# Kernel optimization log

Hardware: AMD Instinct MI355X
Metric: run time of the kernel (lower is better)

The kernel has to match this reference:

```python
import jax, jax.numpy as jnp
import numpy as np
import math

# Model dims (match init_kwargs)
H = 4096      # hidden_size
NH = 32       # num attention heads
NKV = 8       # num kv heads
D = 128       # head_dim
S = 2048      # num tokens
WINDOW = 1024 # sliding window (layer_idx=0 -> active)
SCALE = D ** -0.5
# YaRN rope params from GptOssConfig.rope_parameters
BASE = 500000.0
FACTOR = 4.0
ORIG_MAX = 32768
BETA_FAST = 32
BETA_SLOW = 1


def _yarn_cos_sin(positions):
    """YaRN-scaled rotary cos/sin, NEOX style. Returns ([S, D/2], [S, D/2])."""
    d2 = D // 2
    pos_freqs = BASE ** (np.arange(d2, dtype=np.float64) * 2.0 / D)
    inv_extra = 1.0 / pos_freqs
    inv_inter = 1.0 / (FACTOR * pos_freqs)

    def corr_dim(n):
        return (D * math.log(ORIG_MAX / (n * 2 * math.pi))) / (2 * math.log(BASE))

    low = max(math.floor(corr_dim(BETA_FAST)), 0)
    high = min(math.ceil(corr_dim(BETA_SLOW)), d2 - 1)
    ramp = np.clip((np.arange(d2, dtype=np.float64) - low) / max(high - low, 0.001), 0.0, 1.0)
    mask = 1.0 - ramp  # 1 -> extrapolation (high freq), 0 -> interpolation (low freq)
    inv_freq = inv_inter * (1.0 - mask) + inv_extra * mask
    mscale = 0.1 * math.log(FACTOR) + 1.0
    freqs = positions.astype(jnp.float32)[:, None] * jnp.asarray(inv_freq, dtype=jnp.float32)[None, :]
    return jnp.cos(freqs) * mscale, jnp.sin(freqs) * mscale


def _rope(x, cos, sin):
    # x: [S, h, D]; rotate-halves (NEOX)
    x1, x2 = jnp.split(x, 2, axis=-1)
    c, s = cos[:, None, :], sin[:, None, :]
    return jnp.concatenate([x1 * c - x2 * s, x2 * c + x1 * s], axis=-1)


def reference(hidden_states, positions, qkv_w, qkv_b, o_w, o_b, sinks):
    qs, kvs = NH * D, NKV * D
    qkv = hidden_states @ qkv_w.T + qkv_b                  # [S, qs + 2*kvs]
    q = qkv[:, :qs].reshape(S, NH, D)
    k = qkv[:, qs:qs + kvs].reshape(S, NKV, D)
    v = qkv[:, qs + kvs:].reshape(S, NKV, D)

    cos, sin = _yarn_cos_sin(positions)
    q = _rope(q, cos, sin)
    k = _rope(k, cos, sin)

    # GQA: expand kv heads to match q heads
    g = NH // NKV
    k = jnp.repeat(k, g, axis=1)                            # [S, NH, D]
    v = jnp.repeat(v, g, axis=1)

    scores = jnp.einsum('qhd,khd->hqk', q, k) * SCALE       # [NH, S, S]
    i = jnp.arange(S)[:, None]
    j = jnp.arange(S)[None, :]
    allowed = (j <= i) & ((i - j) < WINDOW)                 # causal + sliding window
    scores = jnp.where(allowed[None, :, :], scores, -jnp.inf)

    # sink-aware softmax: learned per-head sink logit joins the normalization
    m = jnp.maximum(jnp.max(scores, axis=-1), sinks[:, None])   # [NH, S]
    e = jnp.exp(scores - m[..., None])                          # masked -> exp(-inf)=0
    denom = e.sum(-1) + jnp.exp(sinks[:, None] - m)             # [NH, S]
    probs = e / denom[..., None]

    attn = jnp.einsum('hqk,khd->qhd', probs, v).reshape(S, NH * D)
    return attn @ o_w.T + o_b


def setup_inputs() -> dict:
    key = jax.random.key(0)
    k1, k2, k3, k4, k5 = jax.random.split(key, 5)
    w_scale = 0.02
    return {
        'hidden_states': jax.random.normal(k1, (S, H), dtype=jnp.float32),
        'positions': jnp.arange(S, dtype=jnp.int64) if jax.config.jax_enable_x64 else jnp.arange(S, dtype=jnp.int32),
        'qkv_w': jax.random.normal(k2, (NH * D + 2 * NKV * D, H), dtype=jnp.float32) * w_scale,
        'qkv_b': jax.random.normal(k3, (NH * D + 2 * NKV * D,), dtype=jnp.float32) * w_scale,
        'o_w': jax.random.normal(k4, (H, H), dtype=jnp.float32) * w_scale,
        'o_b': jax.random.normal(k5, (H,), dtype=jnp.float32) * w_scale,
        'sinks': jnp.zeros((NH,), dtype=jnp.float32),
    }
```

## Files before the change

kernel.cpp:

```cpp
#include <hip/hip_runtime.h>

#define S_LEN   2048
#define HID     4096
#define NH      32
#define NKV     8
#define HD      128
#define QKV_N   (NH*HD + 2*NKV*HD)
#define WINDOW  1024

typedef unsigned short u16;
typedef short s8v  __attribute__((ext_vector_type(8)));
typedef short s4v  __attribute__((ext_vector_type(4)));
typedef float f4v  __attribute__((ext_vector_type(4)));

#define MFMA16x32(a, b, c) __builtin_amdgcn_mfma_f32_16x16x32_bf16(a, b, c, 0, 0, 0)

typedef __attribute__((address_space(1))) const unsigned int g_u32;
typedef __attribute__((address_space(3))) unsigned int l_u32;

__device__ __forceinline__ float bf2f(u16 h) {
  union { unsigned int u; float f; } x;
  x.u = ((unsigned int)h) << 16;
  return x.f;
}
__device__ __forceinline__ u16 f2bf(float f) {
  union { float f; unsigned int u; } x;
  x.f = f;
  unsigned int u = x.u;
  return (u16)((u + 0x7FFFu + ((u >> 16) & 1u)) >> 16);
}

__global__ __launch_bounds__(256) void cvt_bf16(const float* __restrict__ in,
                                               u16* __restrict__ out) {
  int i = (blockIdx.x * 256 + threadIdx.x) * 4;
  float4 v = *(const float4*)&in[i];
  u16 h[4] = { f2bf(v.x), f2bf(v.y), f2bf(v.z), f2bf(v.w) };
  *(s4v*)&out[i] = *(const s4v*)h;
}

template<int OUT_BF16>
__global__ __launch_bounds__(512, 2) void gemm_bt(
    const u16* __restrict__ A, const u16* __restrict__ B,
    const float* __restrict__ bias, void* __restrict__ Cp,
    int M, int N, int K)
{
  __shared__ __align__(16) char lds[3 * 49152];
  const int tid  = threadIdx.x;
  const int lane = tid & 63;
  const int w    = tid >> 6;
  const int wm   = w >> 2, wn = w & 3;
  const int ln   = lane & 15, quad = lane >> 4;
  const long mBase = (long)blockIdx.y * 128;
  const long nBase = (long)blockIdx.x * 256;
  const u16* Ab = A + mBase * (long)K;
  const u16* Bb = B + nBase * (long)K;
  const long rs = (long)K * 2;

  f4v acc[4][4];
#pragma unroll
  for (int i = 0; i < 4; ++i)
#pragma unroll
    for (int j = 0; j < 4; ++j)
#pragma unroll
      for (int r = 0; r < 4; ++r) acc[i][j][r] = 0.0f;

  const int nt = K >> 6;

  auto stage = [&](int tile) {
    char* base = lds + (tile % 3) * 49152;
    const int ktb = tile * 128;
#pragma unroll
    for (int k = 0; k < 6; ++k) {
      const u16* gsrc = (k < 2) ? Ab : Bb;
      char* ldst      = (k < 2) ? base : (base + 16384);
      const int kk    = (k < 2) ? k : (k - 2);
      int o  = kk * 8192 + w * 1024 + lane * 16;
      int o2 = o ^ ((o >> 3) & 0x70);
      const char* gp = (const char*)gsrc + (long)(o2 >> 7) * rs + ktb + (o2 & 127);
      __builtin_amdgcn_global_load_lds((g_u32*)(const void*)gp,
                                       (l_u32*)(void*)(ldst + kk * 8192 + w * 1024),
                                       16, 0, 0);
    }
  };

  stage(0);
  stage(1);
  asm volatile("s_waitcnt vmcnt(6)" ::: "memory");
  __builtin_amdgcn_s_barrier();
  __builtin_amdgcn_sched_barrier(0);

  int bsel = 0;
  for (int t = 0; t < nt; ++t) {
    char* base = lds + bsel * 49152;
    if (t + 2 < nt) stage(t + 2);

    __builtin_amdgcn_s_setprio(1);
#pragma unroll
    for (int ks = 0; ks < 2; ++ks) {
      s8v af[4], bf[4];
#pragma unroll
      for (int f = 0; f < 4; ++f) {
        int r = wm * 64 + f * 16 + ln;
        int o = r * 128 + ks * 64 + quad * 16;
        o ^= (r & 7) << 4;
        af[f] = *(const s8v*)(base + o);
      }
#pragma unroll
      for (int j = 0; j < 4; ++j) {
        int r = wn * 64 + j * 16 + ln;
        int o = r * 128 + ks * 64 + quad * 16;
        o ^= (r & 7) << 4;
        bf[j] = *(const s8v*)(base + 16384 + o);
      }
#pragma unroll
      for (int i = 0; i < 4; ++i)
#pragma unroll
        for (int j = 0; j < 4; ++j)
          acc[i][j] = MFMA16x32(af[i], bf[j], acc[i][j]);
    }
    __builtin_amdgcn_s_setprio(0);

    if (t < nt - 2) {
      asm volatile("s_waitcnt vmcnt(6)" ::: "memory");
      __builtin_amdgcn_s_barrier();
      __builtin_amdgcn_sched_barrier(0);
    } else if (t == nt - 2) {
      asm volatile("s_waitcnt vmcnt(0)" ::: "memory");
      __builtin_amdgcn_s_barrier();
      __builtin_amdgcn_sched_barrier(0);
    }
    bsel = (bsel == 2) ? 0 : bsel + 1;
  }

#pragma unroll
  for (int i = 0; i < 4; ++i) {
    long rowb = mBase + wm * 64 + i * 16 + quad * 4;
#pragma unroll
    for (int j = 0; j < 4; ++j) {
      long col = nBase + wn * 64 + j * 16 + ln;
      float bv = bias[col];
#pragma unroll
      for (int r = 0; r < 4; ++r) {
        float v = acc[i][j][r] + bv;
        if (OUT_BF16) ((u16*)Cp)[(rowb + r) * (long)N + col] = f2bf(v);
        else          ((float*)Cp)[(rowb + r) * (long)N + col] = v;
      }
    }
  }
}

__global__ __launch_bounds__(256) void rope_split(
    const u16* __restrict__ qkv, const int* __restrict__ positions,
    u16* __restrict__ qo, u16* __restrict__ ko, u16* __restrict__ vo)
{
  const int s = blockIdx.x;
  const int t = threadIdx.x;
  __shared__ float csh[64], snh[64];

  if (t < 64) {
    const double LN_BASE = log(500000.0);
    const double TWO_PI  = 6.283185307179586476925287;
    double cf  = 128.0 * log(32768.0 / (32.0 * TWO_PI)) / (2.0 * LN_BASE);
    double cs_ = 128.0 * log(32768.0 / TWO_PI) / (2.0 * LN_BASE);
    double lowd  = floor(cf);  if (lowd < 0.0)  lowd = 0.0;
    double highd = ceil(cs_);  if (highd > 63.0) highd = 63.0;
    double denom = highd - lowd; if (denom < 0.001) denom = 0.001;
    double d = (double)t;
    double inv_extra = exp(-LN_BASE * d / 64.0);
    double inv_inter = inv_extra * 0.25;
    double ramp = (d - lowd) / denom;
    ramp = ramp < 0.0 ? 0.0 : (ramp > 1.0 ? 1.0 : ramp);
    double maskv = 1.0 - ramp;
    double invf = inv_inter * (1.0 - maskv) + inv_extra * maskv;
    float freq = (float)positions[s] * (float)invf;
    const float msc = 1.1386294361119891f;
    csh[t] = cosf(freq) * msc;
    snh[t] = sinf(freq) * msc;
  }
  __syncthreads();

  const u16* row = qkv + (size_t)s * QKV_N;
  const float SC = 0.08838834764831845f;

#pragma unroll
  for (int i = 0; i < 8; ++i) {
    int p = i * 256 + t;
    int hh = p >> 6, d = p & 63;
    float x1 = bf2f(row[hh * 128 + d]), x2 = bf2f(row[hh * 128 + d + 64]);
    float c = csh[d], sn = snh[d];
    qo[(size_t)s * 4096 + hh * 128 + d]      = f2bf((x1 * c - x2 * sn) * SC);
    qo[(size_t)s * 4096 + hh * 128 + d + 64] = f2bf((x2 * c + x1 * sn) * SC);
  }
#pragma unroll
  for (int i = 0; i < 2; ++i) {
    int p = i * 256 + t;
    int hh = p >> 6, d = p & 63;
    float x1 = bf2f(row[4096 + hh * 128 + d]), x2 = bf2f(row[4096 + hh * 128 + d + 64]);
    float c = csh[d], sn = snh[d];
    ko[(size_t)s * 1024 + hh * 128 + d]      = f2bf(x1 * c - x2 * sn);
    ko[(size_t)s * 1024 + hh * 128 + d + 64] = f2bf(x2 * c + x1 * sn);
  }
#pragma unroll
  for (int i = 0; i < 4; ++i) {
    int e = i * 256 + t;
    vo[(size_t)s * 1024 + e] = row[5120 + e];
  }
}

__global__ __launch_bounds__(256) void transpose_v(const u16* __restrict__ vb,
                                                   u16* __restrict__ vt) {
  __shared__ u16 tile[64][72];
  const int s0 = blockIdx.x * 64, c0 = blockIdx.y * 64;
  const int tid = threadIdx.x;
#pragma unroll
  for (int t = 0; t < 2; ++t) {
    int row = t * 32 + (tid >> 3), col = (tid & 7) * 8;
    *(s8v*)&tile[row][col] = *(const s8v*)&vb[(size_t)(s0 + row) * 1024 + c0 + col];
  }
  __syncthreads();
#pragma unroll
  for (int t = 0; t < 2; ++t) {
    int orow = t * 32 + (tid >> 3), ocol = (tid & 7) * 8;
    u16 v[8];
#pragma unroll
    for (int e = 0; e < 8; ++e) v[e] = tile[ocol + e][orow];
    *(s8v*)&vt[(size_t)(c0 + orow) * 2048 + s0 + ocol] = *(const s8v*)v;
  }
}

__global__ __launch_bounds__(256) void attn_fwd(
    const u16* __restrict__ Q, const u16* __restrict__ Kb,
    const u16* __restrict__ Vt, const float* __restrict__ sinks,
    u16* __restrict__ O)
{
  const int h = blockIdx.y, kvh = h >> 2;
  const int q0 = blockIdx.x * 64;
  const int tid = threadIdx.x, w = tid >> 6, lane = tid & 63;
  const int ln = lane & 15, quad = lane >> 4;
  const int qw = q0 + w * 16;
  const int qi = qw + ln;

  __shared__ __align__(16) u16 sK[64 * 136];
  __shared__ __align__(16) u16 sVt[128 * 72];
  __shared__ __align__(16) u16 sP[4][16 * 72];

  s8v qf[4];
  {
    const u16* qrow = Q + (size_t)qi * 4096 + h * 128;
#pragma unroll
    for (int kb = 0; kb < 4; ++kb)
      qf[kb] = *(const s8v*)&qrow[kb * 32 + quad * 8];
  }

  float m_v = sinks[h], l_v = 1.0f;
  f4v accO[8];
#pragma unroll
  for (int j = 0; j < 8; ++j)
#pragma unroll
    for (int r = 0; r < 4; ++r) accO[j][r] = 0.0f;

  int lo = q0 - (WINDOW - 1); if (lo < 0) lo = 0; lo &= ~63;

  for (int kt = lo; kt <= q0; kt += 64) {
    __syncthreads();
#pragma unroll
    for (int t = 0; t < 4; ++t) {
      int c = t * 256 + tid;
      int row = c >> 4, col = (c & 15) * 8;
      *(s8v*)&sK[row * 136 + col] =
          *(const s8v*)&Kb[(size_t)(kt + row) * 1024 + kvh * 128 + col];
    }
#pragma unroll
    for (int t = 0; t < 4; ++t) {
      int c = t * 256 + tid;
      int row = c >> 3, col = (c & 7) * 8;
      *(s8v*)&sVt[row * 72 + col] =
          *(const s8v*)&Vt[(size_t)(kvh * 128 + row) * 2048 + kt + col];
    }
    __syncthreads();

    f4v sc[4];
    bool dead[4];
#pragma unroll
    for (int h4 = 0; h4 < 4; ++h4) {
      const int kb16 = kt + h4 * 16;
      dead[h4] = (kb16 > qw + 15) || (kb16 + 15 < qw - (WINDOW - 1));
      if (dead[h4]) {
#pragma unroll
        for (int r = 0; r < 4; ++r) sc[h4][r] = -1e30f;
        continue;
      }
      f4v s;
#pragma unroll
      for (int r = 0; r < 4; ++r) s[r] = 0.0f;
#pragma unroll
      for (int kb = 0; kb < 4; ++kb) {
        s8v kf = *(const s8v*)&sK[(h4 * 16 + ln) * 136 + kb * 32 + quad * 8];
        s = MFMA16x32(kf, qf[kb], s);
      }
      const bool full = (kb16 + 15 <= qw) && (qw + 15 - kb16 <= WINDOW - 1);
      if (!full) {
        int base = qi - kb16 - quad * 4;
#pragma unroll
        for (int r = 0; r < 4; ++r)
          s[r] = ((unsigned)(base - r) <= (WINDOW - 1)) ? s[r] : -1e30f;
      }
      sc[h4] = s;
    }

    float mn = m_v;
#pragma unroll
    for (int h4 = 0; h4 < 4; ++h4)
#pragma unroll
      for (int r = 0; r < 4; ++r) mn = fmaxf(mn, sc[h4][r]);
    mn = fmaxf(mn, __shfl_xor(mn, 16));
    mn = fmaxf(mn, __shfl_xor(mn, 32));

    float alpha = __expf(m_v - mn);
    m_v = mn;
    l_v *= alpha;
#pragma unroll
    for (int j = 0; j < 8; ++j)
#pragma unroll
      for (int r = 0; r < 4; ++r) accO[j][r] *= alpha;

    float lsum = 0.0f;
#pragma unroll
    for (int h4 = 0; h4 < 4; ++h4) {
      float p[4];
#pragma unroll
      for (int r = 0; r < 4; ++r) p[r] = __expf(sc[h4][r] - mn);
      lsum += (p[0] + p[1]) + (p[2] + p[3]);
      u16 pb[4] = { f2bf(p[0]), f2bf(p[1]), f2bf(p[2]), f2bf(p[3]) };
      *(s4v*)&sP[w][ln * 72 + h4 * 16 + quad * 4] = *(const s4v*)pb;
    }
    lsum += __shfl_xor(lsum, 16);
    lsum += __shfl_xor(lsum, 32);
    l_v += lsum;

    __syncthreads();

#pragma unroll
    for (int c2 = 0; c2 < 2; ++c2) {
      if (dead[2 * c2] && dead[2 * c2 + 1]) continue;
      s8v pf = *(const s8v*)&sP[w][ln * 72 + c2 * 32 + quad * 8];
#pragma unroll
      for (int j = 0; j < 8; ++j) {
        s8v vf = *(const s8v*)&sVt[(j * 16 + ln) * 72 + c2 * 32 + quad * 8];
        accO[j] = MFMA16x32(vf, pf, accO[j]);
      }
    }
  }

  __syncthreads();
  u16* sO = sK;
  const float rl = 1.0f / l_v;
#pragma unroll
  for (int j = 0; j < 8; ++j) {
    u16 ob[4] = { f2bf(accO[j][0] * rl), f2bf(accO[j][1] * rl),
                  f2bf(accO[j][2] * rl), f2bf(accO[j][3] * rl) };
    *(s4v*)&sO[(w * 16 + ln) * 136 + j * 16 + quad * 4] = *(const s4v*)ob;
  }
  __syncthreads();
  {
    int row = lane >> 2, cc = lane & 3;
#pragma unroll
    for (int i = 0; i < 4; ++i) {
      s8v v = *(const s8v*)&sO[(w * 16 + row) * 136 + cc * 8 + i * 32];
      *(s8v*)&O[(size_t)(q0 + w * 16 + row) * 4096 + h * 128 + cc * 8 + i * 32] = v;
    }
  }
}

extern "C" void kernel_launch(void* const* d_in, const int* in_sizes, int n_in,
                              void* d_out, int out_size, void* d_ws, size_t ws_size,
                              hipStream_t stream) {
  const float* hidden    = (const float*)d_in[0];
  const int*   positions = (const int*)d_in[1];
  const float* qkv_w     = (const float*)d_in[2];
  const float* qkv_b     = (const float*)d_in[3];
  const float* o_w       = (const float*)d_in[4];
  const float* o_b       = (const float*)d_in[5];
  const float* sinks     = (const float*)d_in[6];

  char* ws = (char*)d_ws;
  u16* wW   = (u16*)ws;
  u16* qb   = (u16*)ws;
  u16* kb   = (u16*)(ws + 16777216ull);
  u16* vb   = (u16*)(ws + 20971520ull);
  u16* vt   = (u16*)(ws + 25165824ull);
  u16* attn = (u16*)(ws + 29360128ull);
  u16* hb   = (u16*)(ws + 50331648ull);
  u16* qkvb = (u16*)(ws + 67108864ull);
  u16* oWb  = (u16*)(ws + 50331648ull);

  cvt_bf16<<<8192, 256, 0, stream>>>(hidden, hb);
  cvt_bf16<<<24576, 256, 0, stream>>>(qkv_w, wW);

  gemm_bt<1><<<dim3(QKV_N / 256, S_LEN / 128), 512, 0, stream>>>(
      hb, wW, qkv_b, (void*)qkvb, S_LEN, QKV_N, HID);

  rope_split<<<S_LEN, 256, 0, stream>>>(qkvb, positions, qb, kb, vb);

  cvt_bf16<<<16384, 256, 0, stream>>>(o_w, oWb);

  transpose_v<<<dim3(32, 16), 256, 0, stream>>>(vb, vt);

  attn_fwd<<<dim3(S_LEN / 64, NH), 256, 0, stream>>>(qb, kb, vt, sinks, attn);

  gemm_bt<0><<<dim3(HID / 256, S_LEN / 128), 512, 0, stream>>>(
      attn, oWb, o_b, d_out, S_LEN, HID, HID);
}
```

Measured before the change: 517.1 us.

## Halve GEMM K-tile to shrink LDS and fuse input conversion kernels

The GEMM K-tile drops from 64 to 32, cutting the triple-buffered LDS footprint in half. The launch-bound minimum blocks per CU rises from 2 to 4, which raises occupancy at the cost of tighter register limits. The swizzle pattern and wait counts are adjusted to the 64-byte rows. The two fp32-to-bf16 conversion launches for hidden states and QKV weights are merged into one kernel to save a launch. Smaller K tiles mean twice as many barriers per K loop, and a 4-block target may force register spills for the 64-register accumulator.

```diff
diff --git a/kernel.cpp b/kernel.cpp
--- a/kernel.cpp
+++ b/kernel.cpp
@@ -38,13 +38,27 @@
   *(s4v*)&out[i] = *(const s4v*)h;
 }
 
+__global__ __launch_bounds__(256) void cvt_fused(
+    const float* __restrict__ hidden, const float* __restrict__ qkv_w,
+    u16* __restrict__ hb, u16* __restrict__ wW) {
+  int b = blockIdx.x;
+  const float* in;
+  u16* out;
+  int i;
+  if (b < 24576) { in = qkv_w;  out = wW; i = (b * 256 + threadIdx.x) * 4; }
+  else           { in = hidden; out = hb; i = ((b - 24576) * 256 + threadIdx.x) * 4; }
+  float4 v = *(const float4*)&in[i];
+  u16 h[4] = { f2bf(v.x), f2bf(v.y), f2bf(v.z), f2bf(v.w) };
+  *(s4v*)&out[i] = *(const s4v*)h;
+}
+
 template<int OUT_BF16>
-__global__ __launch_bounds__(512, 2) void gemm_bt(
+__global__ __launch_bounds__(512, 4) void gemm_bt(
     const u16* __restrict__ A, const u16* __restrict__ B,
     const float* __restrict__ bias, void* __restrict__ Cp,
     int M, int N, int K)
 {
-  __shared__ __align__(16) char lds[3 * 49152];
+  __shared__ __align__(16) char lds[3 * 24576];
   const int tid  = threadIdx.x;
   const int lane = tid & 63;
   const int w    = tid >> 6;
@@ -64,19 +78,19 @@
 #pragma unroll
       for (int r = 0; r < 4; ++r) acc[i][j][r] = 0.0f;
 
-  const int nt = K >> 6;
+  const int nt = K >> 5;
 
   auto stage = [&](int tile) {
-    char* base = lds + (tile % 3) * 49152;
-    const int ktb = tile * 128;
-#pragma unroll
-    for (int k = 0; k < 6; ++k) {
-      const u16* gsrc = (k < 2) ? Ab : Bb;
-      char* ldst      = (k < 2) ? base : (base + 16384);
-      const int kk    = (k < 2) ? k : (k - 2);
+    char* base = lds + (tile % 3) * 24576;
+    const int ktb = tile * 64;
+#pragma unroll
+    for (int k = 0; k < 3; ++k) {
+      const u16* gsrc = (k == 0) ? Ab : Bb;
+      char* ldst      = (k == 0) ? base : (base + 8192);
+      const int kk    = (k == 0) ? 0 : (k - 1);
       int o  = kk * 8192 + w * 1024 + lane * 16;
-      int o2 = o ^ ((o >> 3) & 0x70);
-      const char* gp = (const char*)gsrc + (long)(o2 >> 7) * rs + ktb + (o2 & 127);
+      int o2 = o ^ ((o >> 3) & 0x30);
+      const char* gp = (const char*)gsrc + (long)(o2 >> 6) * rs + ktb + (o2 & 63);
       __builtin_amdgcn_global_load_lds((g_u32*)(const void*)gp,
                                        (l_u32*)(void*)(ldst + kk * 8192 + w * 1024),
                                        16, 0, 0);
@@ -85,43 +99,40 @@
 
   stage(0);
   stage(1);
-  asm volatile("s_waitcnt vmcnt(6)" ::: "memory");
+  asm volatile("s_waitcnt vmcnt(3)" ::: "memory");
   __builtin_amdgcn_s_barrier();
   __builtin_amdgcn_sched_barrier(0);
 
   int bsel = 0;
   for (int t = 0; t < nt; ++t) {
-    char* base = lds + bsel * 49152;
+    char* base = lds + bsel * 24576;
     if (t + 2 < nt) stage(t + 2);
 
     __builtin_amdgcn_s_setprio(1);
-#pragma unroll
-    for (int ks = 0; ks < 2; ++ks) {
-      s8v af[4], bf[4];
-#pragma unroll
-      for (int f = 0; f < 4; ++f) {
-        int r = wm * 64 + f * 16 + ln;
-        int o = r * 128 + ks * 64 + quad * 16;
-        o ^= (r & 7) << 4;
-        af[f] = *(const s8v*)(base + o);
-      }
-#pragma unroll
-      for (int j = 0; j < 4; ++j) {
-        int r = wn * 64 + j * 16 + ln;
-        int o = r * 128 + ks * 64 + quad * 16;
-        o ^= (r & 7) << 4;
-        bf[j] = *(const s8v*)(base + 16384 + o);
-      }
-#pragma unroll
-      for (int i = 0; i < 4; ++i)
-#pragma unroll
-        for (int j = 0; j < 4; ++j)
-          acc[i][j] = MFMA16x32(af[i], bf[j], acc[i][j]);
-    }
+    s8v af[4], bf[4];
+#pragma unroll
+    for (int f = 0; f < 4; ++f) {
+      int r = wm * 64 + f * 16 + ln;
+      int o = r * 64 + quad * 16;
+      o ^= (o >> 3) & 0x30;
+      af[f] = *(const s8v*)(base + o);
+    }
+#pragma unroll
+    for (int j = 0; j < 4; ++j) {
+      int r = wn * 64 + j * 16 + ln;
+      int o = r * 64 + quad * 16;
+      o ^= (o >> 3) & 0x30;
+      bf[j] = *(const s8v*)(base + 8192 + o);
+    }
+#pragma unroll
+    for (int i = 0; i < 4; ++i)
+#pragma unroll
+      for (int j = 0; j < 4; ++j)
+        acc[i][j] = MFMA16x32(af[i], bf[j], acc[i][j]);
     __builtin_amdgcn_s_setprio(0);
 
     if (t < nt - 2) {
-      asm volatile("s_waitcnt vmcnt(6)" ::: "memory");
+      asm volatile("s_waitcnt vmcnt(3)" ::: "memory");
       __builtin_amdgcn_s_barrier();
       __builtin_amdgcn_sched_barrier(0);
     } else if (t == nt - 2) {
@@ -394,8 +405,7 @@
   u16* qkvb = (u16*)(ws + 67108864ull);
   u16* oWb  = (u16*)(ws + 50331648ull);
 
-  cvt_bf16<<<8192, 256, 0, stream>>>(hidden, hb);
-  cvt_bf16<<<24576, 256, 0, stream>>>(qkv_w, wW);
+  cvt_fused<<<32768, 256, 0, stream>>>(hidden, qkv_w, hb, wW);
 
   gemm_bt<1><<<dim3(QKV_N / 256, S_LEN / 128), 512, 0, stream>>>(
       hb, wW, qkv_b, (void*)qkvb, S_LEN, QKV_N, HID);
```

Result: no change. 511.7 us (-1.0%).
